# Performance work log

Hardware: AMD Instinct MI355X
Metric: run time of the kernel (lower is better)

## Reference

```python
import jax, jax.numpy as jnp
import numpy as np

B, T, D, H, DFF = 2, 2048, 1024, 16, 4096
DK = D // H
EPS = 1e-12
NEG = -1e9

def _ln(x, g, b):
    m = jnp.mean(x, axis=-1, keepdims=True)
    v = jnp.mean((x - m) ** 2, axis=-1, keepdims=True)
    return (x - m) / jnp.sqrt(v + EPS) * g + b

def setup_inputs() -> dict:
    key = jax.random.key(0)
    ks = jax.random.split(key, 8)
    s = 0.02
    return {
        "x": jax.random.normal(ks[0], (B, T, D), jnp.float32),
        "mask": jnp.ones((1, 1, T, T), jnp.int32),
        "wq": jax.random.normal(ks[1], (D, D), jnp.float32) * s,
        "bq": jnp.zeros((D,), jnp.float32),
        "wk": jax.random.normal(ks[2], (D, D), jnp.float32) * s,
        "bk": jnp.zeros((D,), jnp.float32),
        "wv": jax.random.normal(ks[3], (D, D), jnp.float32) * s,
        "bv": jnp.zeros((D,), jnp.float32),
        "wo": jax.random.normal(ks[4], (D, D), jnp.float32) * s,
        "bo": jnp.zeros((D,), jnp.float32),
        "w1": jax.random.normal(ks[5], (DFF, D), jnp.float32) * s,
        "b1": jnp.zeros((DFF,), jnp.float32),
        "w2": jax.random.normal(ks[6], (D, DFF), jnp.float32) * s,
        "b2": jnp.zeros((D,), jnp.float32),
        "g1": jnp.ones((D,), jnp.float32),
        "beta1": jnp.zeros((D,), jnp.float32),
        "g2": jnp.ones((D,), jnp.float32),
        "beta2": jnp.zeros((D,), jnp.float32),
    }

def reference(x, mask, wq, bq, wk, bk, wv, bv, wo, bo, w1, b1, w2, b2, g1, beta1, g2, beta2):
    # pre-norm (note: residual taken from ln1 output, faithful to source)
    xn = _ln(x, g1, beta1)
    # torch Linear: y = x @ W.T + b
    def proj(w, b):
        return (jnp.einsum('btd,ed->bte', xn, w) + b).reshape(B, T, H, DK).transpose(0, 2, 1, 3)
    q = proj(wq, bq)  # [B,H,T,DK]
    k = proj(wk, bk)
    v = proj(wv, bv)
    scores = jnp.einsum('bhqd,bhkd->bhqk', q, k) / jnp.sqrt(jnp.float32(DK))
    scores = jnp.where(mask == 0, jnp.float32(NEG), scores)
    weights = jax.nn.softmax(scores, axis=-1)  # dropout is identity in eval
    att = jnp.einsum('bhqk,bhkd->bhqd', weights, v)
    att = att.transpose(0, 2, 1, 3).reshape(B, T, D)
    h = jnp.einsum('btd,ed->bte', att, wo) + bo
    x = xn + h
    x = _ln(x, g2, beta2)
    ff = jax.nn.relu(jnp.einsum('btd,fd->btf', x, w1) + b1)
    ff = jnp.einsum('btf,df->btd', ff, w2) + b2
    return x + ff
```

## Files before the change

kernel.cpp:

```cpp
#include <hip/hip_runtime.h>

typedef unsigned short u16;
typedef __attribute__((ext_vector_type(8))) short short8;
typedef __attribute__((ext_vector_type(4))) float f32x4;
typedef __attribute__((ext_vector_type(4))) unsigned short u16x4;
typedef __attribute__((ext_vector_type(2))) unsigned int u32x2;

#define DEV static __device__ __forceinline__

DEV u16 f2b(float f) {
    unsigned int u = __builtin_bit_cast(unsigned int, f);
    u += 0x7FFFu + ((u >> 16) & 1u);
    return (u16)(u >> 16);
}
DEV float b2f(u16 v) {
    unsigned int u = ((unsigned int)v) << 16;
    return __builtin_bit_cast(float, u);
}
DEV void gload16(const void* g, void* l) {
    __builtin_amdgcn_global_load_lds((const __attribute__((address_space(1))) void*)g,
                                     (__attribute__((address_space(3))) void*)l,
                                     16, 0, 0);
}
DEV unsigned int cvt_pk(float lo, float hi) {
    unsigned int r;
    asm("v_cvt_pk_bf16_f32 %0, %1, %2" : "=v"(r) : "v"(lo), "v"(hi));
    return r;
}

static constexpr float KSCALE = 0.18033688011112042f;

__global__ __launch_bounds__(256) void cvt_bf16_k(const float* __restrict__ s,
                                                  u16* __restrict__ d, int n4) {
    int i = blockIdx.x * 256 + threadIdx.x;
    if (i >= n4) return;
    float4 v = ((const float4*)s)[i];
    u16x4 o;
    o[0] = f2b(v.x); o[1] = f2b(v.y); o[2] = f2b(v.z); o[3] = f2b(v.w);
    ((u16x4*)d)[i] = o;
}

template <int INTYPE>
__global__ __launch_bounds__(256) void ln_k(const void* __restrict__ in,
                                            const float* __restrict__ g,
                                            const float* __restrict__ be,
                                            u16* __restrict__ outb) {
    int row = blockIdx.x;
    int t = threadIdx.x;
    float v[4];
    if constexpr (INTYPE == 0) {
        float4 x = ((const float4*)((const float*)in + (size_t)row * 1024))[t];
        v[0] = x.x; v[1] = x.y; v[2] = x.z; v[3] = x.w;
    } else {
        u16x4 x = ((const u16x4*)((const u16*)in + (size_t)row * 1024))[t];
#pragma unroll
        for (int i = 0; i < 4; i++) v[i] = b2f(x[i]);
    }
    float s = v[0] + v[1] + v[2] + v[3];
    float s2 = v[0] * v[0] + v[1] * v[1] + v[2] * v[2] + v[3] * v[3];
#pragma unroll
    for (int off = 1; off < 64; off <<= 1) {
        s += __shfl_xor(s, off);
        s2 += __shfl_xor(s2, off);
    }
    __shared__ float red[8];
    int wid = t >> 6, lane = t & 63;
    if (lane == 0) { red[wid] = s; red[4 + wid] = s2; }
    __syncthreads();
    float S = red[0] + red[1] + red[2] + red[3];
    float S2 = red[4] + red[5] + red[6] + red[7];
    float mean = S * (1.f / 1024.f);
    float var = fmaxf(S2 * (1.f / 1024.f) - mean * mean, 0.f);
    float rinv = rsqrtf(var + 1e-12f);
    float4 gv = ((const float4*)g)[t];
    float4 bv = ((const float4*)be)[t];
    u16x4 o;
    o[0] = f2b((v[0] - mean) * rinv * gv.x + bv.x);
    o[1] = f2b((v[1] - mean) * rinv * gv.y + bv.y);
    o[2] = f2b((v[2] - mean) * rinv * gv.z + bv.z);
    o[3] = f2b((v[3] - mean) * rinv * gv.w + bv.w);
    ((u16x4*)(outb + (size_t)row * 1024))[t] = o;
}

template <int EPI, int BM>
__global__ __launch_bounds__(256) void gemm_bt(
    const u16* __restrict__ A, const u16* __restrict__ Bw,
    const float* __restrict__ b0, const float* __restrict__ b1,
    const float* __restrict__ b2, u16* __restrict__ outb,
    float* __restrict__ outf, const u16* __restrict__ res,
    u16* __restrict__ vt, int M, int N, int K) {
    constexpr int MFR = BM / 32;
    constexpr int BS = (BM + 128) * 32;
    __shared__ u16 SB[3 * BS];
    int tid = threadIdx.x, wid = tid >> 6, lane = tid & 63;
    int l15 = lane & 15, l4 = lane >> 4;
    int m0 = blockIdx.y * BM, n0 = blockIdx.x * 128;
    int wr = wid >> 1, wc = wid & 1;

    f32x4 acc[MFR][4] = {};

    int srow = tid >> 2;
    int scol = (tid & 3) * 8;
    const u16* Ag  = A  + (size_t)(m0 + srow) * K + scol;
    const u16* Ag2 = Ag + (size_t)64 * K;
    const u16* Bg  = Bw + (size_t)(n0 + srow) * K + scol;
    const u16* Bg2 = Bg + (size_t)64 * K;
    int ldst = wid * 1024;

    auto stage = [&](int t, int bufi) {
        char* base = (char*)SB + (size_t)bufi * (BS * 2);
        size_t ko = (size_t)t * 32;
        gload16(Ag + ko, base + ldst);
        if constexpr (BM == 128) gload16(Ag2 + ko, base + 4096 + ldst);
        gload16(Bg + ko, base + BM * 64 + ldst);
        gload16(Bg2 + ko, base + BM * 64 + 4096 + ldst);
    };

    const int NT = K >> 5;
    stage(0, 0);
    stage(1, 1);

    int cb = 0;
    for (int i = 0; i < NT; ++i) {
        if (i == NT - 1) {
            asm volatile("s_waitcnt vmcnt(0)" ::: "memory");
        } else if constexpr (BM == 128) {
            asm volatile("s_waitcnt vmcnt(4)" ::: "memory");
        } else {
            asm volatile("s_waitcnt vmcnt(3)" ::: "memory");
        }
        __builtin_amdgcn_s_barrier();
        __builtin_amdgcn_sched_barrier(0);
        int sb = cb + 2; if (sb >= 3) sb -= 3;
        if (i + 2 < NT) stage(i + 2, sb);

        const u16* Abuf = SB + (size_t)cb * BS;
        const u16* Bbuf = Abuf + BM * 32;
        short8 af[MFR], bfr[4];
        const u16* ap = &Abuf[(wr * (BM / 2) + l15) * 32 + l4 * 8];
        const u16* bp = &Bbuf[(wc * 64 + l15) * 32 + l4 * 8];
#pragma unroll
        for (int i2 = 0; i2 < MFR; i2++) af[i2] = *(const short8*)(ap + i2 * 512);
#pragma unroll
        for (int i2 = 0; i2 < 4; i2++) bfr[i2] = *(const short8*)(bp + i2 * 512);
#pragma unroll
        for (int mi = 0; mi < MFR; mi++)
#pragma unroll
            for (int ni = 0; ni < 4; ni++)
                acc[mi][ni] = __builtin_amdgcn_mfma_f32_16x16x32_bf16(
                    af[mi], bfr[ni], acc[mi][ni], 0, 0, 0);
        cb = (cb == 2) ? 0 : cb + 1;
    }

    int mbase = m0 + wr * (BM / 2);
    int nbase = n0 + wc * 64;
#pragma unroll
    for (int mi = 0; mi < MFR; mi++) {
#pragma unroll
        for (int ni = 0; ni < 4; ni++) {
            int n = nbase + ni * 16 + l15;
            int mr = mbase + mi * 16 + l4 * 4;
            if constexpr (EPI == 0) {
                if (n < 2048) {
                    float bias = (n < 1024) ? b0[n] : b1[n - 1024];
                    float scale = (n < 1024) ? 1.f : KSCALE;
#pragma unroll
                    for (int i = 0; i < 4; i++)
                        outb[(size_t)(mr + i) * 2048 + n] =
                            f2b((acc[mi][ni][i] + bias) * scale);
                } else {
                    float bias = b2[n - 2048];
                    int bidx = m0 >> 11;
                    int tb = mr & 2047;
                    u16x4 pk;
#pragma unroll
                    for (int i = 0; i < 4; i++) pk[i] = f2b(acc[mi][ni][i] + bias);
                    *(u16x4*)&vt[((size_t)(bidx * 1024 + (n - 2048))) * 2048 + tb] = pk;
                }
            } else if constexpr (EPI == 1) {
                float bias = b0[n];
#pragma unroll
                for (int i = 0; i < 4; i++) {
                    size_t off = (size_t)(mr + i) * N + n;
                    outb[off] = f2b(acc[mi][ni][i] + bias + b2f(res[off]));
                }
            } else if constexpr (EPI == 2) {
                float bias = b0[n];
#pragma unroll
                for (int i = 0; i < 4; i++)
                    outb[(size_t)(mr + i) * N + n] =
                        f2b(fmaxf(acc[mi][ni][i] + bias, 0.f));
            } else {
                float bias = b0[n];
#pragma unroll
                for (int i = 0; i < 4; i++) {
                    size_t off = (size_t)(mr + i) * N + n;
                    outf[off] = acc[mi][ni][i] + bias + b2f(res[off]);
                }
            }
        }
    }
}

__global__ __launch_bounds__(512, 4) void attn_k(const u16* __restrict__ qk,
                                                 const u16* __restrict__ vt,
                                                 u16* __restrict__ att) {
    __shared__ u16 K_lds[2][64 * 64];
    __shared__ u16 V_lds[2][64 * 64];
    __shared__ u16 P_lds[8][16 * 64];
    int tid = threadIdx.x, wid = tid >> 6, lane = tid & 63;
    int l15 = lane & 15, l4 = lane >> 4;
    int bh = blockIdx.y, b = bh >> 4, h = bh & 15;
    size_t boff = (size_t)b * 2048;
    size_t hoff = (size_t)b * 1024 + h * 64;
    int q0 = blockIdx.x * 128 + wid * 16;

    short8 qf[2];
    {
        const u16* qb = qk + (boff + q0 + l15) * 2048 + h * 64 + l4 * 8;
        qf[0] = *(const short8*)(qb);
        qf[1] = *(const short8*)(qb + 32);
    }
    f32x4 o_acc[4] = {};
    float m = -1e30f, lsum = 0.f;
    char* Pw = (char*)&P_lds[wid][0];

    int srow = tid >> 3, scs = (tid & 7) ^ (srow & 7);
    const u16* Kg = qk + (boff + srow) * 2048 + 1024 + h * 64 + scs * 8;
    const u16* Vg = vt + (hoff + srow) * 2048 + scs * 8;
    int ldst = wid * 1024;

    auto stage = [&](char* kb, char* vb, int tile) {
        gload16(Kg + (size_t)tile * 131072, kb + ldst);
        gload16(Vg + tile * 64, vb + ldst);
    };

    stage((char*)&K_lds[0][0], (char*)&V_lds[0][0], 0);

    for (int kt = 0; kt < 32; ++kt) {
        int cur = kt & 1;
        const u16* Kl = cur ? &K_lds[1][0] : &K_lds[0][0];
        const u16* Vl = cur ? &V_lds[1][0] : &V_lds[0][0];
        char* Kn = cur ? (char*)&K_lds[0][0] : (char*)&K_lds[1][0];
        char* Vn = cur ? (char*)&V_lds[0][0] : (char*)&V_lds[1][0];
        stage(Kn, Vn, (kt + 1) & 31);
        asm volatile("s_waitcnt vmcnt(2)" ::: "memory");
        __builtin_amdgcn_s_barrier();
        __builtin_amdgcn_sched_barrier(0);

        f32x4 s_acc[4] = {};
        {
            short8 kf[4][2];
#pragma unroll
            for (int kvt = 0; kvt < 4; kvt++) {
                int row = kvt * 16 + l15;
#pragma unroll
                for (int kc = 0; kc < 2; kc++) {
                    int ch = (kc * 4 + l4) ^ (row & 7);
                    kf[kvt][kc] = *(const short8*)&Kl[row * 64 + ch * 8];
                }
            }
#pragma unroll
            for (int kvt = 0; kvt < 4; kvt++)
#pragma unroll
                for (int kc = 0; kc < 2; kc++)
                    s_acc[kvt] = __builtin_amdgcn_mfma_f32_16x16x32_bf16(
                        kf[kvt][kc], qf[kc], s_acc[kvt], 0, 0, 0);
        }

        float tm = s_acc[0][0];
#pragma unroll
        for (int kvt = 0; kvt < 4; kvt++)
#pragma unroll
            for (int r = 0; r < 4; r++) tm = fmaxf(tm, s_acc[kvt][r]);
        tm = fmaxf(tm, __shfl_xor(tm, 16));
        tm = fmaxf(tm, __shfl_xor(tm, 32));
        bool defer = __all(tm <= m + 8.f);
        if (!defer) {
            float mnew = fmaxf(m, tm);
            float alpha = exp2f(m - mnew);
            m = mnew;
            lsum *= alpha;
#pragma unroll
            for (int dt = 0; dt < 4; dt++)
#pragma unroll
                for (int r = 0; r < 4; r++) o_acc[dt][r] *= alpha;
        }
        float ps = 0.f;
#pragma unroll
        for (int kvt = 0; kvt < 4; kvt++)
#pragma unroll
            for (int r = 0; r < 4; r++) {
                float p = exp2f(s_acc[kvt][r] - m);
                s_acc[kvt][r] = p;
                ps += p;
            }
        ps += __shfl_xor(ps, 16);
        ps += __shfl_xor(ps, 32);
        lsum += ps;

#pragma unroll
        for (int kvt = 0; kvt < 4; kvt++) {
            u32x2 w;
            w[0] = cvt_pk(s_acc[kvt][0], s_acc[kvt][1]);
            w[1] = cvt_pk(s_acc[kvt][2], s_acc[kvt][3]);
            int ch = (kvt * 2 + (l4 >> 1)) ^ (l15 & 7);
            *(u32x2*)(Pw + l15 * 128 + ch * 16 + (l4 & 1) * 8) = w;
        }
        {
            short8 pf[2], vf[4][2];
#pragma unroll
            for (int kc = 0; kc < 2; kc++) {
                int ch = (kc * 4 + l4) ^ (l15 & 7);
                pf[kc] = *(const short8*)(Pw + l15 * 128 + ch * 16);
            }
#pragma unroll
            for (int dt = 0; dt < 4; dt++) {
                int row = dt * 16 + l15;
#pragma unroll
                for (int kc = 0; kc < 2; kc++) {
                    int ch = (kc * 4 + l4) ^ (row & 7);
                    vf[dt][kc] = *(const short8*)&Vl[row * 64 + ch * 8];
                }
            }
#pragma unroll
            for (int dt = 0; dt < 4; dt++)
#pragma unroll
                for (int kc = 0; kc < 2; kc++)
                    o_acc[dt] = __builtin_amdgcn_mfma_f32_16x16x32_bf16(
                        vf[dt][kc], pf[kc], o_acc[dt], 0, 0, 0);
        }
        __builtin_amdgcn_sched_barrier(0);
        __builtin_amdgcn_s_barrier();
    }

    float rl = 1.f / lsum;
#pragma unroll
    for (int dt = 0; dt < 4; dt++) {
        u16x4 o;
#pragma unroll
        for (int r = 0; r < 4; r++) o[r] = f2b(o_acc[dt][r] * rl);
        *(u16x4*)&att[(boff + q0 + l15) * 1024 + h * 64 + dt * 16 + l4 * 4] = o;
    }
}

extern "C" void kernel_launch(void* const* d_in, const int* in_sizes, int n_in,
                              void* d_out, int out_size, void* d_ws, size_t ws_size,
                              hipStream_t stream) {
    (void)in_sizes; (void)n_in; (void)out_size; (void)ws_size;
    const float* x   = (const float*)d_in[0];
    const float* wq  = (const float*)d_in[2];
    const float* bq  = (const float*)d_in[3];
    const float* wk  = (const float*)d_in[4];
    const float* bk  = (const float*)d_in[5];
    const float* wv  = (const float*)d_in[6];
    const float* bv  = (const float*)d_in[7];
    const float* wo  = (const float*)d_in[8];
    const float* bo  = (const float*)d_in[9];
    const float* w1  = (const float*)d_in[10];
    const float* b1  = (const float*)d_in[11];
    const float* w2  = (const float*)d_in[12];
    const float* b2  = (const float*)d_in[13];
    const float* g1  = (const float*)d_in[14];
    const float* be1 = (const float*)d_in[15];
    const float* g2  = (const float*)d_in[16];
    const float* be2 = (const float*)d_in[17];
    float* out = (float*)d_out;

    char* ws = (char*)d_ws;
    u16* wqkv  = (u16*)(ws + (size_t)0);
    u16* wo_b  = (u16*)(ws + ((size_t)6  << 20));
    u16* w1_b  = (u16*)(ws + ((size_t)8  << 20));
    u16* w2_b  = (u16*)(ws + ((size_t)16 << 20));
    u16* xn_b  = (u16*)(ws + ((size_t)24 << 20));
    u16* x2_b  = (u16*)(ws + ((size_t)32 << 20));
    u16* x3_b  = (u16*)(ws + ((size_t)40 << 20));
    u16* qk_b  = (u16*)(ws + ((size_t)48 << 20));
    u16* vt_b  = (u16*)(ws + ((size_t)64 << 20));
    u16* att_b = (u16*)(ws + ((size_t)72 << 20));
    u16* ff_b  = (u16*)(ws + ((size_t)48 << 20));

    cvt_bf16_k<<<1024, 256, 0, stream>>>(wq, wqkv,               1024 * 1024 / 4);
    cvt_bf16_k<<<1024, 256, 0, stream>>>(wk, wqkv + 1024 * 1024, 1024 * 1024 / 4);
    cvt_bf16_k<<<1024, 256, 0, stream>>>(wv, wqkv + 2048 * 1024, 1024 * 1024 / 4);
    cvt_bf16_k<<<1024, 256, 0, stream>>>(wo, wo_b, 1024 * 1024 / 4);
    cvt_bf16_k<<<4096, 256, 0, stream>>>(w1, w1_b, 4096 * 1024 / 4);
    cvt_bf16_k<<<4096, 256, 0, stream>>>(w2, w2_b, 4096 * 1024 / 4);
    ln_k<0><<<4096, 256, 0, stream>>>(x, g1, be1, xn_b);
    gemm_bt<0, 128><<<dim3(24, 32), 256, 0, stream>>>(
        xn_b, wqkv, bq, bk, bv, qk_b, nullptr, nullptr, vt_b, 4096, 3072, 1024);
    attn_k<<<dim3(16, 32), 512, 0, stream>>>(qk_b, vt_b, att_b);
    gemm_bt<1, 64><<<dim3(8, 64), 256, 0, stream>>>(
        att_b, wo_b, bo, nullptr, nullptr, x2_b, nullptr, xn_b, nullptr,
        4096, 1024, 1024);
    ln_k<1><<<4096, 256, 0, stream>>>(x2_b, g2, be2, x3_b);
    gemm_bt<2, 128><<<dim3(32, 32), 256, 0, stream>>>(
        x3_b, w1_b, b1, nullptr, nullptr, ff_b, nullptr, nullptr, nullptr,
        4096, 4096, 1024);
    gemm_bt<3, 64><<<dim3(8, 64), 256, 0, stream>>>(
        ff_b, w2_b, b2, nullptr, nullptr, nullptr, out, x3_b, nullptr,
        4096, 1024, 4096);
}
```

Before: 260.8 us.

## Shrink attention blocks to four waves and compute row sums via MFMA

The attention kernel now runs 256-thread blocks covering 64 queries each, launched on twice as many blocks. Each thread issues two async loads per K/V tile instead of one, and the loop is unrolled by two to drop the buffer-select logic. The softmax denominator now comes from an MFMA against a ones vector over the bf16 P fragments, replacing the exp sum and its shuffle reductions. The running max starts at zero and the max reduction uses a tree. This aims to raise occupancy and cut VALU work, but each K/V tile is reused by fewer queries, so global traffic per query rises, and the row sum now uses bf16-rounded probabilities.

Result: no change. 260.4 us (-0.1%).

```diff
diff --git a/kernel.cpp b/kernel.cpp
--- a/kernel.cpp
+++ b/kernel.cpp
@@ -202,18 +202,92 @@
     }
 }
 
-__global__ __launch_bounds__(512, 4) void attn_k(const u16* __restrict__ qk,
+#define ATT_STAGE(KN, VN, TILE) do {                                          \
+    size_t koff_ = (size_t)(TILE) * 64 * 2048;                                \
+    gload16(Kg + koff_, (char*)(KN) + ldst);                                  \
+    gload16(Kg + koff_ + 32 * 2048, (char*)(KN) + 4096 + ldst);               \
+    gload16(Vg + (TILE) * 64, (char*)(VN) + ldst);                            \
+    gload16(Vg + (TILE) * 64 + 32 * 2048, (char*)(VN) + 4096 + ldst);         \
+} while (0)
+
+#define ATT_BODY(KL, VL, PRE, WAITSTR) do {                                   \
+    PRE;                                                                      \
+    asm volatile("s_waitcnt " WAITSTR ::: "memory");                          \
+    __builtin_amdgcn_s_barrier();                                             \
+    __builtin_amdgcn_sched_barrier(0);                                        \
+    f32x4 s_acc[4] = {};                                                      \
+    {                                                                         \
+        _Pragma("unroll")                                                     \
+        for (int kvt = 0; kvt < 4; kvt++) {                                   \
+            int row = kvt * 16 + l15;                                         \
+            short8 kf0 = *(const short8*)&(KL)[row * 64 + ((l4) ^ (row & 7)) * 8]; \
+            short8 kf1 = *(const short8*)&(KL)[row * 64 + ((4 + l4) ^ (row & 7)) * 8]; \
+            s_acc[kvt] = __builtin_amdgcn_mfma_f32_16x16x32_bf16(             \
+                kf0, qf[0], s_acc[kvt], 0, 0, 0);                             \
+            s_acc[kvt] = __builtin_amdgcn_mfma_f32_16x16x32_bf16(             \
+                kf1, qf[1], s_acc[kvt], 0, 0, 0);                             \
+        }                                                                     \
+    }                                                                         \
+    float t0 = fmaxf(fmaxf(s_acc[0][0], s_acc[0][1]), s_acc[0][2]);           \
+    float t1 = fmaxf(fmaxf(s_acc[0][3], s_acc[1][0]), s_acc[1][1]);           \
+    float t2 = fmaxf(fmaxf(s_acc[1][2], s_acc[1][3]), s_acc[2][0]);           \
+    float t3 = fmaxf(fmaxf(s_acc[2][1], s_acc[2][2]), s_acc[2][3]);           \
+    float t4 = fmaxf(fmaxf(s_acc[3][0], s_acc[3][1]), s_acc[3][2]);           \
+    float tm = fmaxf(fmaxf(fmaxf(t0, t1), t2),                                \
+                     fmaxf(fmaxf(t3, t4), s_acc[3][3]));                      \
+    tm = fmaxf(tm, __shfl_xor(tm, 16));                                       \
+    tm = fmaxf(tm, __shfl_xor(tm, 32));                                       \
+    if (!__all(tm <= m + 8.f)) {      \
+        float mnew = fmaxf(m, tm);                                            \
+        float alpha = exp2f(m - mnew);                                        \
+        m = mnew;                                                             \
+        _Pragma("unroll")                                                     \
+        for (int dt = 0; dt < 4; dt++)                                        \
+            _Pragma("unroll")                                                 \
+            for (int r = 0; r < 4; r++) o_acc[dt][r] *= alpha;                \
+        _Pragma("unroll")                                                     \
+        for (int r = 0; r < 4; r++) o_sum[r] *= alpha;                        \
+    }                                                                         \
+    _Pragma("unroll")                                                         \
+    for (int kvt = 0; kvt < 4; kvt++) {                                       \
+        u32x2 w;                                                              \
+        w[0] = cvt_pk(exp2f(s_acc[kvt][0] - m), exp2f(s_acc[kvt][1] - m));    \
+        w[1] = cvt_pk(exp2f(s_acc[kvt][2] - m), exp2f(s_acc[kvt][3] - m));    \
+        int ch = (kvt * 2 + (l4 >> 1)) ^ (l15 & 7);                           \
+        *(u32x2*)(Pw + l15 * 128 + ch * 16 + (l4 & 1) * 8) = w;               \
+    }                                                                         \
+    {                                                                         \
+        short8 pf0 = *(const short8*)(Pw + l15 * 128 + ((l4) ^ (l15 & 7)) * 16); \
+        short8 pf1 = *(const short8*)(Pw + l15 * 128 + ((4 + l4) ^ (l15 & 7)) * 16); \
+        o_sum = __builtin_amdgcn_mfma_f32_16x16x32_bf16(ones, pf0, o_sum, 0, 0, 0); \
+        o_sum = __builtin_amdgcn_mfma_f32_16x16x32_bf16(ones, pf1, o_sum, 0, 0, 0); \
+        _Pragma("unroll")                                                     \
+        for (int dt = 0; dt < 4; dt++) {                                      \
+            int row = dt * 16 + l15;                                          \
+            short8 vf0 = *(const short8*)&(VL)[row * 64 + ((l4) ^ (row & 7)) * 8]; \
+            short8 vf1 = *(const short8*)&(VL)[row * 64 + ((4 + l4) ^ (row & 7)) * 8]; \
+            o_acc[dt] = __builtin_amdgcn_mfma_f32_16x16x32_bf16(              \
+                vf0, pf0, o_acc[dt], 0, 0, 0);                                \
+            o_acc[dt] = __builtin_amdgcn_mfma_f32_16x16x32_bf16(              \
+                vf1, pf1, o_acc[dt], 0, 0, 0);                                \
+        }                                                                     \
+    }                                                                         \
+    __builtin_amdgcn_sched_barrier(0);                                        \
+    __builtin_amdgcn_s_barrier();                                             \
+} while (0)
+
+__global__ __launch_bounds__(256, 4) void attn_k(const u16* __restrict__ qk,
                                                  const u16* __restrict__ vt,
                                                  u16* __restrict__ att) {
     __shared__ u16 K_lds[2][64 * 64];
     __shared__ u16 V_lds[2][64 * 64];
-    __shared__ u16 P_lds[8][16 * 64];
+    __shared__ u16 P_lds[4][16 * 64];
     int tid = threadIdx.x, wid = tid >> 6, lane = tid & 63;
     int l15 = lane & 15, l4 = lane >> 4;
     int bh = blockIdx.y, b = bh >> 4, h = bh & 15;
     size_t boff = (size_t)b * 2048;
     size_t hoff = (size_t)b * 1024 + h * 64;
-    int q0 = blockIdx.x * 128 + wid * 16;
+    int q0 = blockIdx.x * 64 + wid * 16;
 
     short8 qf[2];
     {
@@ -221,8 +295,13 @@
         qf[0] = *(const short8*)(qb);
         qf[1] = *(const short8*)(qb + 32);
     }
+    short8 ones;
+#pragma unroll
+    for (int j = 0; j < 8; j++) ones[j] = (short)0x3F80;
+
     f32x4 o_acc[4] = {};
-    float m = -1e30f, lsum = 0.f;
+    f32x4 o_sum = {};
+    float m = 0.f;
     char* Pw = (char*)&P_lds[wid][0];
 
     int srow = tid >> 3, scs = (tid & 7) ^ (srow & 7);
@@ -230,111 +309,18 @@
     const u16* Vg = vt + (hoff + srow) * 2048 + scs * 8;
     int ldst = wid * 1024;
 
-    auto stage = [&](char* kb, char* vb, int tile) {
-        gload16(Kg + (size_t)tile * 131072, kb + ldst);
-        gload16(Vg + tile * 64, vb + ldst);
-    };
-
-    stage((char*)&K_lds[0][0], (char*)&V_lds[0][0], 0);
-
-    for (int kt = 0; kt < 32; ++kt) {
-        int cur = kt & 1;
-        const u16* Kl = cur ? &K_lds[1][0] : &K_lds[0][0];
-        const u16* Vl = cur ? &V_lds[1][0] : &V_lds[0][0];
-        char* Kn = cur ? (char*)&K_lds[0][0] : (char*)&K_lds[1][0];
-        char* Vn = cur ? (char*)&V_lds[0][0] : (char*)&V_lds[1][0];
-        stage(Kn, Vn, (kt + 1) & 31);
-        asm volatile("s_waitcnt vmcnt(2)" ::: "memory");
-        __builtin_amdgcn_s_barrier();
-        __builtin_amdgcn_sched_barrier(0);
-
-        f32x4 s_acc[4] = {};
-        {
-            short8 kf[4][2];
-#pragma unroll
-            for (int kvt = 0; kvt < 4; kvt++) {
-                int row = kvt * 16 + l15;
-#pragma unroll
-                for (int kc = 0; kc < 2; kc++) {
-                    int ch = (kc * 4 + l4) ^ (row & 7);
-                    kf[kvt][kc] = *(const short8*)&Kl[row * 64 + ch * 8];
-                }
-            }
-#pragma unroll
-            for (int kvt = 0; kvt < 4; kvt++)
-#pragma unroll
-                for (int kc = 0; kc < 2; kc++)
-                    s_acc[kvt] = __builtin_amdgcn_mfma_f32_16x16x32_bf16(
-                        kf[kvt][kc], qf[kc], s_acc[kvt], 0, 0, 0);
-        }
-
-        float tm = s_acc[0][0];
-#pragma unroll
-        for (int kvt = 0; kvt < 4; kvt++)
-#pragma unroll
-            for (int r = 0; r < 4; r++) tm = fmaxf(tm, s_acc[kvt][r]);
-        tm = fmaxf(tm, __shfl_xor(tm, 16));
-        tm = fmaxf(tm, __shfl_xor(tm, 32));
-        bool defer = __all(tm <= m + 8.f);
-        if (!defer) {
-            float mnew = fmaxf(m, tm);
-            float alpha = exp2f(m - mnew);
-            m = mnew;
-            lsum *= alpha;
-#pragma unroll
-            for (int dt = 0; dt < 4; dt++)
-#pragma unroll
-                for (int r = 0; r < 4; r++) o_acc[dt][r] *= alpha;
-        }
-        float ps = 0.f;
-#pragma unroll
-        for (int kvt = 0; kvt < 4; kvt++)
-#pragma unroll
-            for (int r = 0; r < 4; r++) {
-                float p = exp2f(s_acc[kvt][r] - m);
-                s_acc[kvt][r] = p;
-                ps += p;
-            }
-        ps += __shfl_xor(ps, 16);
-        ps += __shfl_xor(ps, 32);
-        lsum += ps;
-
-#pragma unroll
-        for (int kvt = 0; kvt < 4; kvt++) {
-            u32x2 w;
-            w[0] = cvt_pk(s_acc[kvt][0], s_acc[kvt][1]);
-            w[1] = cvt_pk(s_acc[kvt][2], s_acc[kvt][3]);
-            int ch = (kvt * 2 + (l4 >> 1)) ^ (l15 & 7);
-            *(u32x2*)(Pw + l15 * 128 + ch * 16 + (l4 & 1) * 8) = w;
-        }
-        {
-            short8 pf[2], vf[4][2];
-#pragma unroll
-            for (int kc = 0; kc < 2; kc++) {
-                int ch = (kc * 4 + l4) ^ (l15 & 7);
-                pf[kc] = *(const short8*)(Pw + l15 * 128 + ch * 16);
-            }
-#pragma unroll
-            for (int dt = 0; dt < 4; dt++) {
-                int row = dt * 16 + l15;
-#pragma unroll
-                for (int kc = 0; kc < 2; kc++) {
-                    int ch = (kc * 4 + l4) ^ (row & 7);
-                    vf[dt][kc] = *(const short8*)&Vl[row * 64 + ch * 8];
-                }
-            }
-#pragma unroll
-            for (int dt = 0; dt < 4; dt++)
-#pragma unroll
-                for (int kc = 0; kc < 2; kc++)
-                    o_acc[dt] = __builtin_amdgcn_mfma_f32_16x16x32_bf16(
-                        vf[dt][kc], pf[kc], o_acc[dt], 0, 0, 0);
-        }
-        __builtin_amdgcn_sched_barrier(0);
-        __builtin_amdgcn_s_barrier();
-    }
-
-    float rl = 1.f / lsum;
+    ATT_STAGE(&K_lds[0][0], &V_lds[0][0], 0);
+    for (int kt2 = 0; kt2 < 15; kt2++) {
+        ATT_BODY(&K_lds[0][0], &V_lds[0][0],
+                 ATT_STAGE(&K_lds[1][0], &V_lds[1][0], 2 * kt2 + 1), "vmcnt(4)");
+        ATT_BODY(&K_lds[1][0], &V_lds[1][0],
+                 ATT_STAGE(&K_lds[0][0], &V_lds[0][0], 2 * kt2 + 2), "vmcnt(4)");
+    }
+    ATT_BODY(&K_lds[0][0], &V_lds[0][0],
+             ATT_STAGE(&K_lds[1][0], &V_lds[1][0], 31), "vmcnt(4)");
+    ATT_BODY(&K_lds[1][0], &V_lds[1][0], ((void)0), "vmcnt(0)");
+
+    float rl = 1.f / o_sum[0];
 #pragma unroll
     for (int dt = 0; dt < 4; dt++) {
         u16x4 o;
@@ -389,7 +375,7 @@
     ln_k<0><<<4096, 256, 0, stream>>>(x, g1, be1, xn_b);
     gemm_bt<0, 128><<<dim3(24, 32), 256, 0, stream>>>(
         xn_b, wqkv, bq, bk, bv, qk_b, nullptr, nullptr, vt_b, 4096, 3072, 1024);
-    attn_k<<<dim3(16, 32), 512, 0, stream>>>(qk_b, vt_b, att_b);
+    attn_k<<<dim3(32, 32), 256, 0, stream>>>(qk_b, vt_b, att_b);
     gemm_bt<1, 64><<<dim3(8, 64), 256, 0, stream>>>(
         att_b, wo_b, bo, nullptr, nullptr, x2_b, nullptr, xn_b, nullptr,
         4096, 1024, 1024);
```

## Split attention KV range across waves with direct register loads and cross-wave combine

Applied to the files above, without the earlier changes.

Attention now uses 256-thread blocks of 32 queries. Each of the four waves handles a quarter of the keys, loading K and V straight from global memory into registers with a software double buffer in place of LDS staging and block barriers. Row sums of P are computed with an MFMA against a ones vector, and the per-wave partial outputs, maxima and sums are merged through LDS at the end. This removes per-tile barriers and gives more blocks, at the cost of more global K/V traffic because each block rereads the full K/V, plus a combine step and higher register pressure.

Result: slower. 308.7 us (+18.4%).

```diff
diff --git a/kernel.cpp b/kernel.cpp
--- a/kernel.cpp
+++ b/kernel.cpp
@@ -202,145 +202,176 @@
     }
 }
 
-__global__ __launch_bounds__(512, 4) void attn_k(const u16* __restrict__ qk,
+__global__ __launch_bounds__(256, 2) void attn_k(const u16* __restrict__ qk,
                                                  const u16* __restrict__ vt,
                                                  u16* __restrict__ att) {
-    __shared__ u16 K_lds[2][64 * 64];
-    __shared__ u16 V_lds[2][64 * 64];
-    __shared__ u16 P_lds[8][16 * 64];
+    __shared__ __align__(16) char smem[34816];
     int tid = threadIdx.x, wid = tid >> 6, lane = tid & 63;
     int l15 = lane & 15, l4 = lane >> 4;
     int bh = blockIdx.y, b = bh >> 4, h = bh & 15;
     size_t boff = (size_t)b * 2048;
     size_t hoff = (size_t)b * 1024 + h * 64;
-    int q0 = blockIdx.x * 128 + wid * 16;
-
-    short8 qf[2];
+    int q0 = blockIdx.x * 32;
+
+    short8 qf[2][2];
+#pragma unroll
+    for (int qfi = 0; qfi < 2; qfi++)
+#pragma unroll
+        for (int kc = 0; kc < 2; kc++)
+            qf[qfi][kc] = *(const short8*)(qk +
+                (boff + q0 + qfi * 16 + l15) * 2048 + h * 64 + kc * 32 + l4 * 8);
+
+    short8 ones;
+#pragma unroll
+    for (int j = 0; j < 8; j++) ones[j] = (short)0x3F80;
+
+    f32x4 o_acc[4][2] = {};
+    f32x4 o_sum[2] = {};
+    float m[2] = {0.f, 0.f};
+    char* Pw0 = smem + (wid * 2 + 0) * 2048;
+    char* Pw1 = smem + (wid * 2 + 1) * 2048;
+
+    const u16* Kb = qk + (boff + wid * 512 + l15) * 2048 + 1024 + h * 64 + l4 * 8;
+    const u16* Vb = vt + (hoff + l15) * 2048 + wid * 512 + l4 * 8;
+
+    short8 kf[2][4][2];
+#pragma unroll
+    for (int kvt = 0; kvt < 4; kvt++)
+#pragma unroll
+        for (int kc = 0; kc < 2; kc++)
+            kf[0][kvt][kc] = *(const short8*)(Kb + kvt * 16 * 2048 + kc * 32);
+
+#pragma unroll
+    for (int kt = 0; kt < 8; ++kt) {
+        const int cu = kt & 1, nx = cu ^ 1;
+        short8 vf[4][2];
+#pragma unroll
+        for (int dt = 0; dt < 4; dt++)
+#pragma unroll
+            for (int kc = 0; kc < 2; kc++)
+                vf[dt][kc] = *(const short8*)(Vb + (size_t)dt * 16 * 2048 +
+                                              kt * 64 + kc * 32);
+        f32x4 s_acc[4][2] = {};
+#pragma unroll
+        for (int kvt = 0; kvt < 4; kvt++)
+#pragma unroll
+            for (int kc = 0; kc < 2; kc++)
+#pragma unroll
+                for (int qfi = 0; qfi < 2; qfi++)
+                    s_acc[kvt][qfi] = __builtin_amdgcn_mfma_f32_16x16x32_bf16(
+                        kf[cu][kvt][kc], qf[qfi][kc], s_acc[kvt][qfi], 0, 0, 0);
+        if (kt < 7) {
+#pragma unroll
+            for (int kvt = 0; kvt < 4; kvt++)
+#pragma unroll
+                for (int kc = 0; kc < 2; kc++)
+                    kf[nx][kvt][kc] = *(const short8*)(Kb +
+                        (size_t)(kt + 1) * 64 * 2048 + kvt * 16 * 2048 + kc * 32);
+        }
+#pragma unroll
+        for (int qfi = 0; qfi < 2; qfi++) {
+            float t0 = fmaxf(fmaxf(s_acc[0][qfi][0], s_acc[0][qfi][1]), s_acc[0][qfi][2]);
+            float t1 = fmaxf(fmaxf(s_acc[0][qfi][3], s_acc[1][qfi][0]), s_acc[1][qfi][1]);
+            float t2 = fmaxf(fmaxf(s_acc[1][qfi][2], s_acc[1][qfi][3]), s_acc[2][qfi][0]);
+            float t3 = fmaxf(fmaxf(s_acc[2][qfi][1], s_acc[2][qfi][2]), s_acc[2][qfi][3]);
+            float t4 = fmaxf(fmaxf(s_acc[3][qfi][0], s_acc[3][qfi][1]), s_acc[3][qfi][2]);
+            float tm = fmaxf(fmaxf(fmaxf(t0, t1), t2),
+                             fmaxf(fmaxf(t3, t4), s_acc[3][qfi][3]));
+            tm = fmaxf(tm, __shfl_xor(tm, 16));
+            tm = fmaxf(tm, __shfl_xor(tm, 32));
+            if (!__all(tm <= m[qfi] + 8.f)) {
+                float mnew = fmaxf(m[qfi], tm);
+                float alpha = exp2f(m[qfi] - mnew);
+                m[qfi] = mnew;
+#pragma unroll
+                for (int dt = 0; dt < 4; dt++)
+#pragma unroll
+                    for (int r = 0; r < 4; r++) o_acc[dt][qfi][r] *= alpha;
+#pragma unroll
+                for (int r = 0; r < 4; r++) o_sum[qfi][r] *= alpha;
+            }
+            char* Pw = qfi ? Pw1 : Pw0;
+#pragma unroll
+            for (int kvt = 0; kvt < 4; kvt++) {
+                u32x2 w;
+                w[0] = cvt_pk(exp2f(s_acc[kvt][qfi][0] - m[qfi]),
+                              exp2f(s_acc[kvt][qfi][1] - m[qfi]));
+                w[1] = cvt_pk(exp2f(s_acc[kvt][qfi][2] - m[qfi]),
+                              exp2f(s_acc[kvt][qfi][3] - m[qfi]));
+                int ch = (kvt * 2 + (l4 >> 1)) ^ (l15 & 7);
+                *(u32x2*)(Pw + l15 * 128 + ch * 16 + (l4 & 1) * 8) = w;
+            }
+        }
+#pragma unroll
+        for (int qfi = 0; qfi < 2; qfi++) {
+            char* Pw = qfi ? Pw1 : Pw0;
+            short8 pf0 = *(const short8*)(Pw + l15 * 128 + ((l4) ^ (l15 & 7)) * 16);
+            short8 pf1 = *(const short8*)(Pw + l15 * 128 + ((4 + l4) ^ (l15 & 7)) * 16);
+            o_sum[qfi] = __builtin_amdgcn_mfma_f32_16x16x32_bf16(
+                ones, pf0, o_sum[qfi], 0, 0, 0);
+            o_sum[qfi] = __builtin_amdgcn_mfma_f32_16x16x32_bf16(
+                ones, pf1, o_sum[qfi], 0, 0, 0);
+#pragma unroll
+            for (int dt = 0; dt < 4; dt++) {
+                o_acc[dt][qfi] = __builtin_amdgcn_mfma_f32_16x16x32_bf16(
+                    vf[dt][0], pf0, o_acc[dt][qfi], 0, 0, 0);
+                o_acc[dt][qfi] = __builtin_amdgcn_mfma_f32_16x16x32_bf16(
+                    vf[dt][1], pf1, o_acc[dt][qfi], 0, 0, 0);
+            }
+        }
+    }
+
+    __syncthreads();
+    float* o_cmb = (float*)smem;
+    float* m_cmb = (float*)(smem + 33792);
+    float* l_cmb = (float*)(smem + 34304);
+#pragma unroll
+    for (int dt = 0; dt < 4; dt++)
+#pragma unroll
+        for (int qfi = 0; qfi < 2; qfi++)
+#pragma unroll
+            for (int r = 0; r < 4; r++)
+                o_cmb[wid * 2112 + (dt * 16 + l4 * 4 + r) * 33 + qfi * 16 + l15] =
+                    o_acc[dt][qfi][r];
+    if (l4 == 0) {
+#pragma unroll
+        for (int qfi = 0; qfi < 2; qfi++) {
+            m_cmb[wid * 32 + qfi * 16 + l15] = m[qfi];
+            l_cmb[wid * 32 + qfi * 16 + l15] = o_sum[qfi][0];
+        }
+    }
+    __syncthreads();
     {
-        const u16* qb = qk + (boff + q0 + l15) * 2048 + h * 64 + l4 * 8;
-        qf[0] = *(const short8*)(qb);
-        qf[1] = *(const short8*)(qb + 32);
-    }
-    f32x4 o_acc[4] = {};
-    float m = -1e30f, lsum = 0.f;
-    char* Pw = (char*)&P_lds[wid][0];
-
-    int srow = tid >> 3, scs = (tid & 7) ^ (srow & 7);
-    const u16* Kg = qk + (boff + srow) * 2048 + 1024 + h * 64 + scs * 8;
-    const u16* Vg = vt + (hoff + srow) * 2048 + scs * 8;
-    int ldst = wid * 1024;
-
-    auto stage = [&](char* kb, char* vb, int tile) {
-        gload16(Kg + (size_t)tile * 131072, kb + ldst);
-        gload16(Vg + tile * 64, vb + ldst);
-    };
-
-    stage((char*)&K_lds[0][0], (char*)&V_lds[0][0], 0);
-
-    for (int kt = 0; kt < 32; ++kt) {
-        int cur = kt & 1;
-        const u16* Kl = cur ? &K_lds[1][0] : &K_lds[0][0];
-        const u16* Vl = cur ? &V_lds[1][0] : &V_lds[0][0];
-        char* Kn = cur ? (char*)&K_lds[0][0] : (char*)&K_lds[1][0];
-        char* Vn = cur ? (char*)&V_lds[0][0] : (char*)&V_lds[1][0];
-        stage(Kn, Vn, (kt + 1) & 31);
-        asm volatile("s_waitcnt vmcnt(2)" ::: "memory");
-        __builtin_amdgcn_s_barrier();
-        __builtin_amdgcn_sched_barrier(0);
-
-        f32x4 s_acc[4] = {};
-        {
-            short8 kf[4][2];
-#pragma unroll
-            for (int kvt = 0; kvt < 4; kvt++) {
-                int row = kvt * 16 + l15;
-#pragma unroll
-                for (int kc = 0; kc < 2; kc++) {
-                    int ch = (kc * 4 + l4) ^ (row & 7);
-                    kf[kvt][kc] = *(const short8*)&Kl[row * 64 + ch * 8];
-                }
+        int q = tid >> 3, dkc = tid & 7;
+        int qi = q >> 4, ql = q & 15;
+        float mw[4], sw[4];
+#pragma unroll
+        for (int w = 0; w < 4; w++) mw[w] = m_cmb[w * 32 + qi * 16 + ql];
+        float M = fmaxf(fmaxf(mw[0], mw[1]), fmaxf(mw[2], mw[3]));
+        float L = 0.f;
+#pragma unroll
+        for (int w = 0; w < 4; w++) {
+            sw[w] = exp2f(mw[w] - M);
+            L += l_cmb[w * 32 + qi * 16 + ql] * sw[w];
+        }
+        float rl = 1.f / L;
+#pragma unroll
+        for (int w = 0; w < 4; w++) sw[w] *= rl;
+        u16* orow = att + (boff + q0 + q) * 1024 + h * 64 + dkc * 8;
+#pragma unroll
+        for (int c = 0; c < 2; c++) {
+            u16x4 o;
+#pragma unroll
+            for (int j = 0; j < 4; j++) {
+                int dk = dkc * 8 + c * 4 + j;
+                float v = o_cmb[dk * 33 + q] * sw[0] +
+                          o_cmb[2112 + dk * 33 + q] * sw[1] +
+                          o_cmb[4224 + dk * 33 + q] * sw[2] +
+                          o_cmb[6336 + dk * 33 + q] * sw[3];
+                o[j] = f2b(v);
             }
-#pragma unroll
-            for (int kvt = 0; kvt < 4; kvt++)
-#pragma unroll
-                for (int kc = 0; kc < 2; kc++)
-                    s_acc[kvt] = __builtin_amdgcn_mfma_f32_16x16x32_bf16(
-                        kf[kvt][kc], qf[kc], s_acc[kvt], 0, 0, 0);
-        }
-
-        float tm = s_acc[0][0];
-#pragma unroll
-        for (int kvt = 0; kvt < 4; kvt++)
-#pragma unroll
-            for (int r = 0; r < 4; r++) tm = fmaxf(tm, s_acc[kvt][r]);
-        tm = fmaxf(tm, __shfl_xor(tm, 16));
-        tm = fmaxf(tm, __shfl_xor(tm, 32));
-        bool defer = __all(tm <= m + 8.f);
-        if (!defer) {
-            float mnew = fmaxf(m, tm);
-            float alpha = exp2f(m - mnew);
-            m = mnew;
-            lsum *= alpha;
-#pragma unroll
-            for (int dt = 0; dt < 4; dt++)
-#pragma unroll
-                for (int r = 0; r < 4; r++) o_acc[dt][r] *= alpha;
-        }
-        float ps = 0.f;
-#pragma unroll
-        for (int kvt = 0; kvt < 4; kvt++)
-#pragma unroll
-            for (int r = 0; r < 4; r++) {
-                float p = exp2f(s_acc[kvt][r] - m);
-                s_acc[kvt][r] = p;
-                ps += p;
-            }
-        ps += __shfl_xor(ps, 16);
-        ps += __shfl_xor(ps, 32);
-        lsum += ps;
-
-#pragma unroll
-        for (int kvt = 0; kvt < 4; kvt++) {
-            u32x2 w;
-            w[0] = cvt_pk(s_acc[kvt][0], s_acc[kvt][1]);
-            w[1] = cvt_pk(s_acc[kvt][2], s_acc[kvt][3]);
-            int ch = (kvt * 2 + (l4 >> 1)) ^ (l15 & 7);
-            *(u32x2*)(Pw + l15 * 128 + ch * 16 + (l4 & 1) * 8) = w;
-        }
-        {
-            short8 pf[2], vf[4][2];
-#pragma unroll
-            for (int kc = 0; kc < 2; kc++) {
-                int ch = (kc * 4 + l4) ^ (l15 & 7);
-                pf[kc] = *(const short8*)(Pw + l15 * 128 + ch * 16);
-            }
-#pragma unroll
-            for (int dt = 0; dt < 4; dt++) {
-                int row = dt * 16 + l15;
-#pragma unroll
-                for (int kc = 0; kc < 2; kc++) {
-                    int ch = (kc * 4 + l4) ^ (row & 7);
-                    vf[dt][kc] = *(const short8*)&Vl[row * 64 + ch * 8];
-                }
-            }
-#pragma unroll
-            for (int dt = 0; dt < 4; dt++)
-#pragma unroll
-                for (int kc = 0; kc < 2; kc++)
-                    o_acc[dt] = __builtin_amdgcn_mfma_f32_16x16x32_bf16(
-                        vf[dt][kc], pf[kc], o_acc[dt], 0, 0, 0);
-        }
-        __builtin_amdgcn_sched_barrier(0);
-        __builtin_amdgcn_s_barrier();
-    }
-
-    float rl = 1.f / lsum;
-#pragma unroll
-    for (int dt = 0; dt < 4; dt++) {
-        u16x4 o;
-#pragma unroll
-        for (int r = 0; r < 4; r++) o[r] = f2b(o_acc[dt][r] * rl);
-        *(u16x4*)&att[(boff + q0 + l15) * 1024 + h * 64 + dt * 16 + l4 * 4] = o;
+            *(u16x4*)(orow + c * 4) = o;
+        }
     }
 }
 
@@ -389,7 +420,7 @@
     ln_k<0><<<4096, 256, 0, stream>>>(x, g1, be1, xn_b);
     gemm_bt<0, 128><<<dim3(24, 32), 256, 0, stream>>>(
         xn_b, wqkv, bq, bk, bv, qk_b, nullptr, nullptr, vt_b, 4096, 3072, 1024);
-    attn_k<<<dim3(16, 32), 512, 0, stream>>>(qk_b, vt_b, att_b);
+    attn_k<<<dim3(64, 32), 256, 0, stream>>>(qk_b, vt_b, att_b);
     gemm_bt<1, 64><<<dim3(8, 64), 256, 0, stream>>>(
         att_b, wo_b, bo, nullptr, nullptr, x2_b, nullptr, xn_b, nullptr,
         4096, 1024, 1024);
```
